# Performance work log

Hardware: AMD Instinct MI355X
Metric: run time of the kernel (lower is better)

Reference implementation:

```python
import jax, jax.numpy as jnp
import numpy as np
import math

B, P = 4096, 512
WDT = 10          # lyr_wdt = number of irreps (multiplicity)
EPS2 = 1e-12      # NormActivation epsilon=1e-6, squared


def setup_inputs() -> dict:
    key = jax.random.key(0)
    ks = jax.random.split(key, 8)
    return {
        "invar_2b": jax.random.normal(ks[0], (B, P, 5), jnp.float32),
        "vectors_2b": jax.random.normal(ks[1], (B, P, 9), jnp.float32),
        # torch.nn.Linear params (stored as [in, out])
        "w1_0": jax.random.normal(ks[2], (5, WDT), jnp.float32) / math.sqrt(5.0),
        "b1_0": jnp.zeros((WDT,), jnp.float32),
        "w1_1": jax.random.normal(ks[3], (WDT, WDT), jnp.float32) / math.sqrt(float(WDT)),
        "b1_1": jnp.zeros((WDT,), jnp.float32),
        # o3.Linear weights (N(0,1) init, e3nn normalizes by sqrt(mul_in) in forward)
        "lin0_w": jax.random.normal(ks[4], (3, WDT), jnp.float32),
        "na0_b": jnp.zeros((WDT,), jnp.float32),   # NormActivation bias
        "lin1_w": jax.random.normal(ks[5], (WDT, WDT), jnp.float32),
        "na1_b": jnp.zeros((WDT,), jnp.float32),
        "final_w": jax.random.normal(ks[6], (WDT, 1), jnp.float32),
    }


def _self_intrc(x, w, bias):
    """o3.Linear (mul_in x 1o -> mul_out x 1o) + NormActivation(tanh, eps=1e-6, bias).

    x: [B, P, mul_in, 3]
    """
    mul_in = x.shape[-2]
    # single l=1 -> l=1 path; e3nn o3.Linear scales by 1/sqrt(fan_in)
    y = jnp.einsum('bpuc,uw->bpwc', x, w) / jnp.sqrt(jnp.float32(mul_in))
    # NormActivation: norm per irrep, clamped at eps^2 before sqrt
    n = jnp.sqrt(jnp.maximum(jnp.sum(y * y, axis=-1), EPS2))  # [B,P,mul_out]
    s = jnp.tanh(n + bias) / n                                # act(norm+b)/norm
    return y * s[..., None]


def reference(invar_2b, vectors_2b, w1_0, b1_0, w1_1, b1_1,
              lin0_w, na0_b, lin1_w, na1_b, final_w):
    # scalar branch: Linear(5,10) + ReLU, Linear(10,10) + ReLU
    y = jax.nn.relu(invar_2b @ w1_0 + b1_0)
    y = jax.nn.relu(y @ w1_1 + b1_1)              # [B, P, WDT] (10x0e)

    # equivariant branch: two self_intrc blocks on 3x1o -> 10x1o -> 10x1o
    v = vectors_2b.reshape(B, P, 3, 3)            # [B,P,3 irreps,3 comps]
    x = _self_intrc(v, lin0_w, na0_b)             # [B,P,WDT,3]
    x = _self_intrc(x, lin1_w, na1_b)             # [B,P,WDT,3]

    # ElementwiseTensorProduct(10x0e, 10x1o) -> 10x1o: per-irrep scalar gating
    x = y[..., None] * x                          # [B,P,WDT,3]

    # final o3.Linear 10x1o -> 1x1o
    x = jnp.einsum('bpuc,uw->bpwc', x, final_w) / jnp.sqrt(jnp.float32(WDT))
    return jnp.sum(x[..., 0, :], axis=1)          # sum over pairs -> [B, 3]
```

## Files before the change

kernel.cpp:

```cpp
#include <hip/hip_runtime.h>
#include <math.h>

#define BB 4096
#define PP 512
#define WDT 10

typedef float float2v __attribute__((ext_vector_type(2)));

#define PKFMA(a, b, c) __builtin_elementwise_fma(a, b, c)
#define PKMAX(a, b)    __builtin_elementwise_max(a, b)
#define FENCE()        __builtin_amdgcn_sched_barrier(0)

__device__ __forceinline__ float2v bc2(float s) { return (float2v){s, s}; }

__device__ __forceinline__ float fast_tanh(float x) {
    float e = __builtin_amdgcn_exp2f(x * 2.8853900817779268f);
    return 1.0f - 2.0f * __builtin_amdgcn_rcpf(e + 1.0f);
}

__global__ __launch_bounds__(512) void frc_2b_kernel(
    const float* __restrict__ invar,
    const float* __restrict__ vectors,
    const float* __restrict__ w1_0,
    const float* __restrict__ b1_0,
    const float* __restrict__ w1_1,
    const float* __restrict__ b1_1,
    const float* __restrict__ lin0_w,
    const float* __restrict__ na0_b,
    const float* __restrict__ lin1_w,
    const float* __restrict__ na1_b,
    const float* __restrict__ final_w,
    float* __restrict__ out)
{
    __shared__ float red[8][3];

    const int b   = blockIdx.x;
    const int tid = threadIdx.x;

    const float* iv = invar   + ((size_t)b * PP + tid) * 5;
    const float* vv = vectors + ((size_t)b * PP + tid) * 9;
    float in5a[5];
    #pragma unroll
    for (int i = 0; i < 5; ++i) in5a[i] = iv[i];
    float v[9];
    #pragma unroll
    for (int i = 0; i < 9; ++i) v[i] = vv[i];

    const float k3sq  = 0.33333333333333333f;
    const float k3k10 = 0.18257418583505536f;
    const float k10   = 0.31622776601683794f;
    const float2v z2  = {0.f, 0.f};

    float2v yp[5];
    #pragma unroll
    for (int jp = 0; jp < 5; ++jp) yp[jp] = *(const float2v*)(b1_0 + 2 * jp);
    #pragma unroll
    for (int i = 0; i < 5; ++i) {
        const float2v xb = bc2(in5a[i]);
        #pragma unroll
        for (int jp = 0; jp < 5; ++jp) {
            float2v wp = *(const float2v*)(w1_0 + i * WDT + 2 * jp);
            yp[jp] = PKFMA(wp, xb, yp[jp]);
        }
    }
    #pragma unroll
    for (int jp = 0; jp < 5; ++jp) yp[jp] = PKMAX(yp[jp], z2);
    FENCE();

    float2v y2p[5];
    #pragma unroll
    for (int jp = 0; jp < 5; ++jp) y2p[jp] = *(const float2v*)(b1_1 + 2 * jp);
    #pragma unroll
    for (int k = 0; k < 5; ++k) {
        const float2v xb = bc2(yp[k >> 1][k & 1]);
        #pragma unroll
        for (int jp = 0; jp < 5; ++jp) {
            float2v wp = *(const float2v*)(w1_1 + k * WDT + 2 * jp);
            y2p[jp] = PKFMA(wp, xb, y2p[jp]);
        }
    }
    FENCE();
    #pragma unroll
    for (int k = 5; k < WDT; ++k) {
        const float2v xb = bc2(yp[k >> 1][k & 1]);
        #pragma unroll
        for (int jp = 0; jp < 5; ++jp) {
            float2v wp = *(const float2v*)(w1_1 + k * WDT + 2 * jp);
            y2p[jp] = PKFMA(wp, xb, y2p[jp]);
        }
    }
    #pragma unroll
    for (int jp = 0; jp < 5; ++jp) y2p[jp] = PKMAX(y2p[jp], z2);
    FENCE();

    float2v c0p[5], c1p[5], c2p[5];
    #pragma unroll
    for (int jp = 0; jp < 5; ++jp) { c0p[jp] = z2; c1p[jp] = z2; c2p[jp] = z2; }
    #pragma unroll
    for (int u = 0; u < 3; ++u) {
        const float2v b0 = bc2(v[u * 3 + 0]);
        const float2v b1 = bc2(v[u * 3 + 1]);
        const float2v b2 = bc2(v[u * 3 + 2]);
        #pragma unroll
        for (int jp = 0; jp < 5; ++jp) {
            float2v wp = *(const float2v*)(lin0_w + u * WDT + 2 * jp);
            c0p[jp] = PKFMA(wp, b0, c0p[jp]);
            c1p[jp] = PKFMA(wp, b1, c1p[jp]);
            c2p[jp] = PKFMA(wp, b2, c2p[jp]);
        }
    }
    float2v x0p[5], x1p[5], x2p[5];
    #pragma unroll
    for (int jp = 0; jp < 5; ++jp) {
        float2v n2p = PKFMA(c0p[jp], c0p[jp], PKFMA(c1p[jp], c1p[jp], c2p[jp] * c2p[jp]));
        float2v mp  = PKMAX(n2p * bc2(k3sq), bc2(1e-12f));
        float2v nab = *(const float2v*)(na0_b + 2 * jp);
        float fh[2];
        #pragma unroll
        for (int h = 0; h < 2; ++h) {
            float m     = mp[h];
            float inv_n = __builtin_amdgcn_rsqf(m);
            float n     = m * inv_n;
            float t     = fast_tanh(n + nab[h]);
            fh[h] = t * inv_n * k3k10;
        }
        float2v fp = {fh[0], fh[1]};
        x0p[jp] = c0p[jp] * fp;
        x1p[jp] = c1p[jp] * fp;
        x2p[jp] = c2p[jp] * fp;
    }
    FENCE();

    float2v e0p[5], e1p[5], e2p[5];
    #pragma unroll
    for (int jp = 0; jp < 5; ++jp) { e0p[jp] = z2; e1p[jp] = z2; e2p[jp] = z2; }
    #pragma unroll
    for (int u = 0; u < 5; ++u) {
        const float2v b0 = bc2(x0p[u >> 1][u & 1]);
        const float2v b1 = bc2(x1p[u >> 1][u & 1]);
        const float2v b2 = bc2(x2p[u >> 1][u & 1]);
        #pragma unroll
        for (int jp = 0; jp < 5; ++jp) {
            float2v wp = *(const float2v*)(lin1_w + u * WDT + 2 * jp);
            e0p[jp] = PKFMA(wp, b0, e0p[jp]);
            e1p[jp] = PKFMA(wp, b1, e1p[jp]);
            e2p[jp] = PKFMA(wp, b2, e2p[jp]);
        }
    }
    FENCE();
    #pragma unroll
    for (int u = 5; u < WDT; ++u) {
        const float2v b0 = bc2(x0p[u >> 1][u & 1]);
        const float2v b1 = bc2(x1p[u >> 1][u & 1]);
        const float2v b2 = bc2(x2p[u >> 1][u & 1]);
        #pragma unroll
        for (int jp = 0; jp < 5; ++jp) {
            float2v wp = *(const float2v*)(lin1_w + u * WDT + 2 * jp);
            e0p[jp] = PKFMA(wp, b0, e0p[jp]);
            e1p[jp] = PKFMA(wp, b1, e1p[jp]);
            e2p[jp] = PKFMA(wp, b2, e2p[jp]);
        }
    }
    FENCE();

    float2v a0p = z2, a1p = z2, a2p = z2;
    #pragma unroll
    for (int jp = 0; jp < 5; ++jp) {
        float2v n2p = PKFMA(e0p[jp], e0p[jp], PKFMA(e1p[jp], e1p[jp], e2p[jp] * e2p[jp]));
        float2v mp  = PKMAX(n2p, bc2(1e-12f));
        float2v nab = *(const float2v*)(na1_b + 2 * jp);
        float2v fwp = *(const float2v*)(final_w + 2 * jp);
        float gh[2];
        #pragma unroll
        for (int h = 0; h < 2; ++h) {
            float m     = mp[h];
            float inv_n = __builtin_amdgcn_rsqf(m);
            float n     = m * inv_n;
            float t     = fast_tanh(n + nab[h]);
            gh[h] = y2p[jp][h] * t * inv_n * fwp[h];
        }
        float2v gp = {gh[0], gh[1]};
        a0p = PKFMA(e0p[jp], gp, a0p);
        a1p = PKFMA(e1p[jp], gp, a1p);
        a2p = PKFMA(e2p[jp], gp, a2p);
    }
    float acc0 = (a0p[0] + a0p[1]) * k10;
    float acc1 = (a1p[0] + a1p[1]) * k10;
    float acc2 = (a2p[0] + a2p[1]) * k10;

    #pragma unroll
    for (int off = 32; off > 0; off >>= 1) {
        acc0 += __shfl_down(acc0, off, 64);
        acc1 += __shfl_down(acc1, off, 64);
        acc2 += __shfl_down(acc2, off, 64);
    }
    const int wave = tid >> 6;
    if ((tid & 63) == 0) { red[wave][0] = acc0; red[wave][1] = acc1; red[wave][2] = acc2; }
    __syncthreads();
    if (tid == 0) {
        float r0 = 0.f, r1 = 0.f, r2 = 0.f;
        #pragma unroll
        for (int wv = 0; wv < 8; ++wv) { r0 += red[wv][0]; r1 += red[wv][1]; r2 += red[wv][2]; }
        out[b * 3 + 0] = r0;
        out[b * 3 + 1] = r1;
        out[b * 3 + 2] = r2;
    }
}

extern "C" void kernel_launch(void* const* d_in, const int* in_sizes, int n_in,
                              void* d_out, int out_size, void* d_ws, size_t ws_size,
                              hipStream_t stream) {
    const float* invar   = (const float*)d_in[0];
    const float* vectors = (const float*)d_in[1];
    const float* w1_0    = (const float*)d_in[2];
    const float* b1_0    = (const float*)d_in[3];
    const float* w1_1    = (const float*)d_in[4];
    const float* b1_1    = (const float*)d_in[5];
    const float* lin0_w  = (const float*)d_in[6];
    const float* na0_b   = (const float*)d_in[7];
    const float* lin1_w  = (const float*)d_in[8];
    const float* na1_b   = (const float*)d_in[9];
    const float* final_w = (const float*)d_in[10];
    float* out = (float*)d_out;

    frc_2b_kernel<<<BB, 512, 0, stream>>>(invar, vectors, w1_0, b1_0, w1_1, b1_1,
                                          lin0_w, na0_b, lin1_w, na1_b, final_w, out);
}
```

Baseline: 165.8 us.

## Process two pairs per thread with 256-thread blocks

Each thread now computes two pairs (tid and tid+256) instead of one, and the block size drops to 256 threads. Weight loads and broadcasts are shared between the two pairs, and the independent work gives more instruction-level parallelism. In exchange, register pressure roughly doubles and fewer waves are resident to hide latency.

```diff
diff --git a/kernel.cpp b/kernel.cpp
--- a/kernel.cpp
+++ b/kernel.cpp
@@ -18,7 +18,7 @@
     return 1.0f - 2.0f * __builtin_amdgcn_rcpf(e + 1.0f);
 }
 
-__global__ __launch_bounds__(512) void frc_2b_kernel(
+__global__ __launch_bounds__(256) void frc_2b_kernel(
     const float* __restrict__ invar,
     const float* __restrict__ vectors,
     const float* __restrict__ w1_0,
@@ -32,133 +32,151 @@
     const float* __restrict__ final_w,
     float* __restrict__ out)
 {
-    __shared__ float red[8][3];
+    __shared__ float red[4][3];
 
     const int b   = blockIdx.x;
     const int tid = threadIdx.x;
 
-    const float* iv = invar   + ((size_t)b * PP + tid) * 5;
-    const float* vv = vectors + ((size_t)b * PP + tid) * 9;
-    float in5a[5];
-    #pragma unroll
-    for (int i = 0; i < 5; ++i) in5a[i] = iv[i];
-    float v[9];
-    #pragma unroll
-    for (int i = 0; i < 9; ++i) v[i] = vv[i];
+    const float* iv0 = invar   + ((size_t)b * PP + tid) * 5;
+    const float* vv0 = vectors + ((size_t)b * PP + tid) * 9;
+    float in5a[2][5];
+    float v[2][9];
+    #pragma unroll
+    for (int i = 0; i < 5; ++i) { in5a[0][i] = iv0[i]; in5a[1][i] = iv0[256 * 5 + i]; }
+    #pragma unroll
+    for (int i = 0; i < 9; ++i) { v[0][i] = vv0[i]; v[1][i] = vv0[256 * 9 + i]; }
 
     const float k3sq  = 0.33333333333333333f;
     const float k3k10 = 0.18257418583505536f;
     const float k10   = 0.31622776601683794f;
     const float2v z2  = {0.f, 0.f};
 
-    float2v yp[5];
-    #pragma unroll
-    for (int jp = 0; jp < 5; ++jp) yp[jp] = *(const float2v*)(b1_0 + 2 * jp);
+    float2v yp[2][5];
+    #pragma unroll
+    for (int jp = 0; jp < 5; ++jp) {
+        float2v bb = *(const float2v*)(b1_0 + 2 * jp);
+        yp[0][jp] = bb; yp[1][jp] = bb;
+    }
     #pragma unroll
     for (int i = 0; i < 5; ++i) {
-        const float2v xb = bc2(in5a[i]);
         #pragma unroll
         for (int jp = 0; jp < 5; ++jp) {
             float2v wp = *(const float2v*)(w1_0 + i * WDT + 2 * jp);
-            yp[jp] = PKFMA(wp, xb, yp[jp]);
-        }
-    }
-    #pragma unroll
-    for (int jp = 0; jp < 5; ++jp) yp[jp] = PKMAX(yp[jp], z2);
-    FENCE();
-
-    float2v y2p[5];
-    #pragma unroll
-    for (int jp = 0; jp < 5; ++jp) y2p[jp] = *(const float2v*)(b1_1 + 2 * jp);
+            yp[0][jp] = PKFMA(wp, bc2(in5a[0][i]), yp[0][jp]);
+            yp[1][jp] = PKFMA(wp, bc2(in5a[1][i]), yp[1][jp]);
+        }
+    }
+    #pragma unroll
+    for (int pr = 0; pr < 2; ++pr)
+        #pragma unroll
+        for (int jp = 0; jp < 5; ++jp) yp[pr][jp] = PKMAX(yp[pr][jp], z2);
+    FENCE();
+
+    float2v y2p[2][5];
+    #pragma unroll
+    for (int jp = 0; jp < 5; ++jp) {
+        float2v bb = *(const float2v*)(b1_1 + 2 * jp);
+        y2p[0][jp] = bb; y2p[1][jp] = bb;
+    }
     #pragma unroll
     for (int k = 0; k < 5; ++k) {
-        const float2v xb = bc2(yp[k >> 1][k & 1]);
         #pragma unroll
         for (int jp = 0; jp < 5; ++jp) {
             float2v wp = *(const float2v*)(w1_1 + k * WDT + 2 * jp);
-            y2p[jp] = PKFMA(wp, xb, y2p[jp]);
+            y2p[0][jp] = PKFMA(wp, bc2(yp[0][k >> 1][k & 1]), y2p[0][jp]);
+            y2p[1][jp] = PKFMA(wp, bc2(yp[1][k >> 1][k & 1]), y2p[1][jp]);
         }
     }
     FENCE();
     #pragma unroll
     for (int k = 5; k < WDT; ++k) {
-        const float2v xb = bc2(yp[k >> 1][k & 1]);
         #pragma unroll
         for (int jp = 0; jp < 5; ++jp) {
             float2v wp = *(const float2v*)(w1_1 + k * WDT + 2 * jp);
-            y2p[jp] = PKFMA(wp, xb, y2p[jp]);
-        }
-    }
-    #pragma unroll
-    for (int jp = 0; jp < 5; ++jp) y2p[jp] = PKMAX(y2p[jp], z2);
-    FENCE();
-
-    float2v c0p[5], c1p[5], c2p[5];
-    #pragma unroll
-    for (int jp = 0; jp < 5; ++jp) { c0p[jp] = z2; c1p[jp] = z2; c2p[jp] = z2; }
+            y2p[0][jp] = PKFMA(wp, bc2(yp[0][k >> 1][k & 1]), y2p[0][jp]);
+            y2p[1][jp] = PKFMA(wp, bc2(yp[1][k >> 1][k & 1]), y2p[1][jp]);
+        }
+    }
+    #pragma unroll
+    for (int pr = 0; pr < 2; ++pr)
+        #pragma unroll
+        for (int jp = 0; jp < 5; ++jp) y2p[pr][jp] = PKMAX(y2p[pr][jp], z2);
+    FENCE();
+
+    float2v c0p[2][5], c1p[2][5], c2p[2][5];
+    #pragma unroll
+    for (int pr = 0; pr < 2; ++pr)
+        #pragma unroll
+        for (int jp = 0; jp < 5; ++jp) { c0p[pr][jp] = z2; c1p[pr][jp] = z2; c2p[pr][jp] = z2; }
     #pragma unroll
     for (int u = 0; u < 3; ++u) {
-        const float2v b0 = bc2(v[u * 3 + 0]);
-        const float2v b1 = bc2(v[u * 3 + 1]);
-        const float2v b2 = bc2(v[u * 3 + 2]);
         #pragma unroll
         for (int jp = 0; jp < 5; ++jp) {
             float2v wp = *(const float2v*)(lin0_w + u * WDT + 2 * jp);
-            c0p[jp] = PKFMA(wp, b0, c0p[jp]);
-            c1p[jp] = PKFMA(wp, b1, c1p[jp]);
-            c2p[jp] = PKFMA(wp, b2, c2p[jp]);
-        }
-    }
-    float2v x0p[5], x1p[5], x2p[5];
-    #pragma unroll
-    for (int jp = 0; jp < 5; ++jp) {
-        float2v n2p = PKFMA(c0p[jp], c0p[jp], PKFMA(c1p[jp], c1p[jp], c2p[jp] * c2p[jp]));
-        float2v mp  = PKMAX(n2p * bc2(k3sq), bc2(1e-12f));
+            #pragma unroll
+            for (int pr = 0; pr < 2; ++pr) {
+                c0p[pr][jp] = PKFMA(wp, bc2(v[pr][u * 3 + 0]), c0p[pr][jp]);
+                c1p[pr][jp] = PKFMA(wp, bc2(v[pr][u * 3 + 1]), c1p[pr][jp]);
+                c2p[pr][jp] = PKFMA(wp, bc2(v[pr][u * 3 + 2]), c2p[pr][jp]);
+            }
+        }
+    }
+    float2v x0p[2][5], x1p[2][5], x2p[2][5];
+    #pragma unroll
+    for (int jp = 0; jp < 5; ++jp) {
         float2v nab = *(const float2v*)(na0_b + 2 * jp);
-        float fh[2];
-        #pragma unroll
-        for (int h = 0; h < 2; ++h) {
-            float m     = mp[h];
-            float inv_n = __builtin_amdgcn_rsqf(m);
-            float n     = m * inv_n;
-            float t     = fast_tanh(n + nab[h]);
-            fh[h] = t * inv_n * k3k10;
-        }
-        float2v fp = {fh[0], fh[1]};
-        x0p[jp] = c0p[jp] * fp;
-        x1p[jp] = c1p[jp] * fp;
-        x2p[jp] = c2p[jp] * fp;
-    }
-    FENCE();
-
-    float2v e0p[5], e1p[5], e2p[5];
-    #pragma unroll
-    for (int jp = 0; jp < 5; ++jp) { e0p[jp] = z2; e1p[jp] = z2; e2p[jp] = z2; }
+        #pragma unroll
+        for (int pr = 0; pr < 2; ++pr) {
+            float2v n2p = PKFMA(c0p[pr][jp], c0p[pr][jp],
+                          PKFMA(c1p[pr][jp], c1p[pr][jp], c2p[pr][jp] * c2p[pr][jp]));
+            float2v mp  = PKMAX(n2p * bc2(k3sq), bc2(1e-12f));
+            float fh[2];
+            #pragma unroll
+            for (int h = 0; h < 2; ++h) {
+                float m     = mp[h];
+                float inv_n = __builtin_amdgcn_rsqf(m);
+                float n     = m * inv_n;
+                float t     = fast_tanh(n + nab[h]);
+                fh[h] = t * inv_n * k3k10;
+            }
+            float2v fp = {fh[0], fh[1]};
+            x0p[pr][jp] = c0p[pr][jp] * fp;
+            x1p[pr][jp] = c1p[pr][jp] * fp;
+            x2p[pr][jp] = c2p[pr][jp] * fp;
+        }
+    }
+    FENCE();
+
+    float2v e0p[2][5], e1p[2][5], e2p[2][5];
+    #pragma unroll
+    for (int pr = 0; pr < 2; ++pr)
+        #pragma unroll
+        for (int jp = 0; jp < 5; ++jp) { e0p[pr][jp] = z2; e1p[pr][jp] = z2; e2p[pr][jp] = z2; }
     #pragma unroll
     for (int u = 0; u < 5; ++u) {
-        const float2v b0 = bc2(x0p[u >> 1][u & 1]);
-        const float2v b1 = bc2(x1p[u >> 1][u & 1]);
-        const float2v b2 = bc2(x2p[u >> 1][u & 1]);
         #pragma unroll
         for (int jp = 0; jp < 5; ++jp) {
             float2v wp = *(const float2v*)(lin1_w + u * WDT + 2 * jp);
-            e0p[jp] = PKFMA(wp, b0, e0p[jp]);
-            e1p[jp] = PKFMA(wp, b1, e1p[jp]);
-            e2p[jp] = PKFMA(wp, b2, e2p[jp]);
+            #pragma unroll
+            for (int pr = 0; pr < 2; ++pr) {
+                e0p[pr][jp] = PKFMA(wp, bc2(x0p[pr][u >> 1][u & 1]), e0p[pr][jp]);
+                e1p[pr][jp] = PKFMA(wp, bc2(x1p[pr][u >> 1][u & 1]), e1p[pr][jp]);
+                e2p[pr][jp] = PKFMA(wp, bc2(x2p[pr][u >> 1][u & 1]), e2p[pr][jp]);
+            }
         }
     }
     FENCE();
     #pragma unroll
     for (int u = 5; u < WDT; ++u) {
-        const float2v b0 = bc2(x0p[u >> 1][u & 1]);
-        const float2v b1 = bc2(x1p[u >> 1][u & 1]);
-        const float2v b2 = bc2(x2p[u >> 1][u & 1]);
         #pragma unroll
         for (int jp = 0; jp < 5; ++jp) {
             float2v wp = *(const float2v*)(lin1_w + u * WDT + 2 * jp);
-            e0p[jp] = PKFMA(wp, b0, e0p[jp]);
-            e1p[jp] = PKFMA(wp, b1, e1p[jp]);
-            e2p[jp] = PKFMA(wp, b2, e2p[jp]);
+            #pragma unroll
+            for (int pr = 0; pr < 2; ++pr) {
+                e0p[pr][jp] = PKFMA(wp, bc2(x0p[pr][u >> 1][u & 1]), e0p[pr][jp]);
+                e1p[pr][jp] = PKFMA(wp, bc2(x1p[pr][u >> 1][u & 1]), e1p[pr][jp]);
+                e2p[pr][jp] = PKFMA(wp, bc2(x2p[pr][u >> 1][u & 1]), e2p[pr][jp]);
+            }
         }
     }
     FENCE();
@@ -166,23 +184,27 @@
     float2v a0p = z2, a1p = z2, a2p = z2;
     #pragma unroll
     for (int jp = 0; jp < 5; ++jp) {
-        float2v n2p = PKFMA(e0p[jp], e0p[jp], PKFMA(e1p[jp], e1p[jp], e2p[jp] * e2p[jp]));
-        float2v mp  = PKMAX(n2p, bc2(1e-12f));
         float2v nab = *(const float2v*)(na1_b + 2 * jp);
         float2v fwp = *(const float2v*)(final_w + 2 * jp);
-        float gh[2];
-        #pragma unroll
-        for (int h = 0; h < 2; ++h) {
-            float m     = mp[h];
-            float inv_n = __builtin_amdgcn_rsqf(m);
-            float n     = m * inv_n;
-            float t     = fast_tanh(n + nab[h]);
-            gh[h] = y2p[jp][h] * t * inv_n * fwp[h];
-        }
-        float2v gp = {gh[0], gh[1]};
-        a0p = PKFMA(e0p[jp], gp, a0p);
-        a1p = PKFMA(e1p[jp], gp, a1p);
-        a2p = PKFMA(e2p[jp], gp, a2p);
+        #pragma unroll
+        for (int pr = 0; pr < 2; ++pr) {
+            float2v n2p = PKFMA(e0p[pr][jp], e0p[pr][jp],
+                          PKFMA(e1p[pr][jp], e1p[pr][jp], e2p[pr][jp] * e2p[pr][jp]));
+            float2v mp  = PKMAX(n2p, bc2(1e-12f));
+            float gh[2];
+            #pragma unroll
+            for (int h = 0; h < 2; ++h) {
+                float m     = mp[h];
+                float inv_n = __builtin_amdgcn_rsqf(m);
+                float n     = m * inv_n;
+                float t     = fast_tanh(n + nab[h]);
+                gh[h] = y2p[pr][jp][h] * t * inv_n * fwp[h];
+            }
+            float2v gp = {gh[0], gh[1]};
+            a0p = PKFMA(e0p[pr][jp], gp, a0p);
+            a1p = PKFMA(e1p[pr][jp], gp, a1p);
+            a2p = PKFMA(e2p[pr][jp], gp, a2p);
+        }
     }
     float acc0 = (a0p[0] + a0p[1]) * k10;
     float acc1 = (a1p[0] + a1p[1]) * k10;
@@ -200,7 +222,7 @@
     if (tid == 0) {
         float r0 = 0.f, r1 = 0.f, r2 = 0.f;
         #pragma unroll
-        for (int wv = 0; wv < 8; ++wv) { r0 += red[wv][0]; r1 += red[wv][1]; r2 += red[wv][2]; }
+        for (int wv = 0; wv < 4; ++wv) { r0 += red[wv][0]; r1 += red[wv][1]; r2 += red[wv][2]; }
         out[b * 3 + 0] = r0;
         out[b * 3 + 1] = r1;
         out[b * 3 + 2] = r2;
@@ -223,6 +245,6 @@
     const float* final_w = (const float*)d_in[10];
     float* out = (float*)d_out;
 
-    frc_2b_kernel<<<BB, 512, 0, stream>>>(invar, vectors, w1_0, b1_0, w1_1, b1_1,
+    frc_2b_kernel<<<BB, 256, 0, stream>>>(invar, vectors, w1_0, b1_0, w1_1, b1_1,
                                           lin0_w, na0_b, lin1_w, na1_b, final_w, out);
 }
```

New measurement: 166.4 us. Within noise of the previous version (+0.3%).
